# Kernel optimization log

Measured on AMD Instinct MI355X. Metric: run time of the kernel, lower is better.

## Reference

```python
import jax, jax.numpy as jnp
import numpy as np

D_MODEL = 1024
NUM_HEADS = 16
D_K = D_MODEL // NUM_HEADS
B, T = 2, 2048


def setup_inputs() -> dict:
    key = jax.random.key(0)
    ks = jax.random.split(key, 11)
    s = 1.0 / np.sqrt(D_MODEL)
    inp = {
        "q": jax.random.normal(ks[0], (B, T, D_MODEL), jnp.float32),
        "k": jax.random.normal(ks[1], (B, T, D_MODEL), jnp.float32),
        "v": jax.random.normal(ks[2], (B, T, D_MODEL), jnp.float32),
        "mask": jnp.tril(jnp.ones((1, 1, T, T), jnp.int32)),  # causal
        "wq": jax.random.normal(ks[3], (D_MODEL, D_MODEL), jnp.float32) * s,
        "bq": jnp.zeros((D_MODEL,), jnp.float32),
        "wk": jax.random.normal(ks[4], (D_MODEL, D_MODEL), jnp.float32) * s,
        "bk": jnp.zeros((D_MODEL,), jnp.float32),
        "wv": jax.random.normal(ks[5], (D_MODEL, D_MODEL), jnp.float32) * s,
        "bv": jnp.zeros((D_MODEL,), jnp.float32),
        "wo": jax.random.normal(ks[6], (D_MODEL, D_MODEL), jnp.float32) * s,
        "bo": jnp.zeros((D_MODEL,), jnp.float32),
    }
    return inp


def reference(q, k, v, mask, wq, bq, wk, bk, wv, bv, wo, bo):
    Bq, Tq, _ = q.shape
    Tk = k.shape[1]
    # projections, split into heads: (B, H, T, d_k)
    qh = (q @ wq + bq).reshape(Bq, Tq, NUM_HEADS, D_K).transpose(0, 2, 1, 3)
    kh = (k @ wk + bk).reshape(Bq, Tk, NUM_HEADS, D_K).transpose(0, 2, 1, 3)
    vh = (v @ wv + bv).reshape(Bq, Tk, NUM_HEADS, D_K).transpose(0, 2, 1, 3)
    scores = jnp.einsum("bhqd,bhkd->bhqk", qh, kh) / jnp.sqrt(jnp.float32(D_K))
    scores = jnp.where(mask == 0, jnp.float32(-1e9), scores)
    attn = jax.nn.softmax(scores, axis=-1)
    ctx = jnp.einsum("bhqk,bhkd->bhqd", attn, vh)
    ctx = ctx.transpose(0, 2, 1, 3).reshape(Bq, Tq, D_MODEL)
    return ctx @ wo + bo
```

## Files before the change

kernel.cpp:

```cpp
#include <hip/hip_runtime.h>
#include <hip/hip_bf16.h>

#define DM 1024
#define NH 16
#define DK 64
#define TT 2048
#define BATCH 2

typedef __attribute__((ext_vector_type(8))) short bf16x8;
typedef __attribute__((ext_vector_type(4))) float f32x4;
typedef __attribute__((ext_vector_type(4))) unsigned short u16x4;
typedef unsigned short u16;

__device__ inline u16 f2b(float x){ __hip_bfloat16 h = __float2bfloat16(x); return *reinterpret_cast<u16*>(&h); }

__device__ inline void gl_lds16(const u16* g, u16* l) {
  __builtin_amdgcn_global_load_lds(
      (const __attribute__((address_space(1))) unsigned int*)g,
      (__attribute__((address_space(3))) unsigned int*)l, 16, 0, 0);
}

__global__ __launch_bounds__(256) void prep(const float* __restrict__ q, const float* __restrict__ k,
                                            const float* __restrict__ v,
                                            const float* __restrict__ wq, const float* __restrict__ wk,
                                            const float* __restrict__ wv, const float* __restrict__ wo,
                                            u16* __restrict__ qb, u16* __restrict__ kb,
                                            u16* __restrict__ vb, u16* __restrict__ wt) {
  int z = blockIdx.z;
  if (z < 3) {
    const float* src = z==0 ? q : z==1 ? k : v;
    u16* dst = z==0 ? qb : z==1 ? kb : vb;
    size_t i = ((size_t)blockIdx.x*256 + threadIdx.x)*8;
    f32x4 a = *(const f32x4*)(src+i);
    f32x4 b = *(const f32x4*)(src+i+4);
    union { bf16x8 v8; u16 e[8]; } u;
    #pragma unroll
    for (int j=0;j<4;j++){ u.e[j] = f2b(a[j]); u.e[4+j] = f2b(b[j]); }
    *(bf16x8*)(dst+i) = u.v8;
  } else {
    int bx = blockIdx.x;
    if (bx >= 1024) return;
    __shared__ float tile[32][33];
    const float* src = z==3 ? wq : z==4 ? wk : z==5 ? wv : wo;
    u16* dst = wt + (size_t)(z-3)*DM*DM;
    int bxx = bx & 31, byy = bx >> 5;
    int tx = threadIdx.x & 31, ty = threadIdx.x >> 5;
    int x  = bxx*32 + tx;
    int y0 = byy*32 + ty;
    #pragma unroll
    for (int i=0;i<32;i+=8) tile[ty+i][tx] = src[(size_t)(y0+i)*DM + x];
    __syncthreads();
    int xo = byy*32 + tx;
    int yo = bxx*32 + ty;
    #pragma unroll
    for (int i=0;i<32;i+=8) dst[(size_t)(yo+i)*DM + xo] = f2b(tile[tx][ty+i]);
  }
}

__global__ __launch_bounds__(256) void gemm_qkv(const u16* __restrict__ qb, const u16* __restrict__ kb,
                                                const u16* __restrict__ vb, const u16* __restrict__ wt,
                                                const float* __restrict__ bq, const float* __restrict__ bk,
                                                const float* __restrict__ bv,
                                                u16* __restrict__ qh, u16* __restrict__ kh,
                                                u16* __restrict__ vhT) {
  const int z = blockIdx.z;
  const u16* A = z==0 ? qb : z==1 ? kb : vb;
  const u16* W = wt + (size_t)z*DM*DM;
  const float* bias = z==0 ? bq : z==1 ? bk : bv;
  u16* outv = z==0 ? qh : z==1 ? kh : vhT;
  const int mode = (z==2) ? 1 : 0;
  const float oscale = (z==0) ? 0.125f : 1.0f;

  __shared__ u16 As[2][128*32];
  __shared__ u16 Bs[2][128*32];
  const int tid = threadIdx.x, lane = tid & 63, wid = tid >> 6;
  const int li = lane & 15, quad = lane >> 4;
  const int row0 = blockIdx.x*128, col0 = blockIdx.y*128;
  const int wr = wid & 1, wc = wid >> 1;

  f32x4 acc[4][4];
  #pragma unroll
  for (int i=0;i<4;i++)
    #pragma unroll
    for (int j=0;j<4;j++) acc[i][j] = f32x4{0.f,0.f,0.f,0.f};

  const int srow = lane >> 2;
  const int scol = (lane & 3) * 8;

  for (int k0 = 0; k0 < DM; k0 += 64) {
    __syncthreads();
    #pragma unroll
    for (int s=0;s<2;s++)
      #pragma unroll
      for (int c=0;c<2;c++) {
        int ch = wid*2 + c;
        gl_lds16(A + (size_t)(row0 + ch*16 + srow)*DM + k0 + s*32 + scol, As[s] + ch*512);
        gl_lds16(W + (size_t)(col0 + ch*16 + srow)*DM + k0 + s*32 + scol, Bs[s] + ch*512);
      }
    __syncthreads();
    #pragma unroll
    for (int s=0;s<2;s++) {
      bf16x8 a[4], b[4];
      #pragma unroll
      for (int i=0;i<4;i++) a[i] = *(const bf16x8*)&As[s][(wr*64 + i*16 + li)*32 + quad*8];
      #pragma unroll
      for (int j=0;j<4;j++) b[j] = *(const bf16x8*)&Bs[s][(wc*64 + j*16 + li)*32 + quad*8];
      #pragma unroll
      for (int i=0;i<4;i++)
        #pragma unroll
        for (int j=0;j<4;j++)
          acc[i][j] = __builtin_amdgcn_mfma_f32_16x16x32_bf16(a[i], b[j], acc[i][j], 0,0,0);
    }
  }

  #pragma unroll
  for (int j=0;j<4;j++) {
    int col = col0 + wc*64 + j*16 + li;
    float bsv = bias[col];
    #pragma unroll
    for (int i=0;i<4;i++) {
      #pragma unroll
      for (int r=0;r<4;r++) {
        int row = row0 + wr*64 + i*16 + quad*4 + r;
        float vv = (acc[i][j][r] + bsv) * oscale;
        int bb = row >> 11, t = row & (TT-1);
        int hh = col >> 6,  d = col & 63;
        size_t idx = (mode == 0)
          ? ((((size_t)(bb*NH + hh)*TT + t) << 6) + d)
          : ((((size_t)(bb*NH + hh)*DK + d)*TT) + t);
        outv[idx] = f2b(vv);
      }
    }
  }
}

__global__ __launch_bounds__(256) void gemm_out64(const u16* __restrict__ A, const u16* __restrict__ W,
                                                  const float* __restrict__ bias, float* __restrict__ out) {
  __shared__ u16 As[2][128*32];
  __shared__ u16 Bs[2][64*32];
  const int tid = threadIdx.x, lane = tid & 63, wid = tid >> 6;
  const int li = lane & 15, quad = lane >> 4;
  const int row0 = blockIdx.x*128, col0 = blockIdx.y*64;
  const int wr = wid & 1, wc = wid >> 1;

  f32x4 acc[4][2];
  #pragma unroll
  for (int i=0;i<4;i++)
    #pragma unroll
    for (int j=0;j<2;j++) acc[i][j] = f32x4{0.f,0.f,0.f,0.f};

  const int srow = lane >> 2;
  const int scol = (lane & 3) * 8;

  for (int k0 = 0; k0 < DM; k0 += 64) {
    __syncthreads();
    #pragma unroll
    for (int s=0;s<2;s++) {
      #pragma unroll
      for (int c=0;c<2;c++) {
        int ch = wid*2 + c;
        gl_lds16(A + (size_t)(row0 + ch*16 + srow)*DM + k0 + s*32 + scol, As[s] + ch*512);
      }
      gl_lds16(W + (size_t)(col0 + wid*16 + srow)*DM + k0 + s*32 + scol, Bs[s] + wid*512);
    }
    __syncthreads();
    #pragma unroll
    for (int s=0;s<2;s++) {
      bf16x8 a[4], b[2];
      #pragma unroll
      for (int i=0;i<4;i++) a[i] = *(const bf16x8*)&As[s][(wr*64 + i*16 + li)*32 + quad*8];
      #pragma unroll
      for (int j=0;j<2;j++) b[j] = *(const bf16x8*)&Bs[s][(wc*32 + j*16 + li)*32 + quad*8];
      #pragma unroll
      for (int i=0;i<4;i++)
        #pragma unroll
        for (int j=0;j<2;j++)
          acc[i][j] = __builtin_amdgcn_mfma_f32_16x16x32_bf16(a[i], b[j], acc[i][j], 0,0,0);
    }
  }

  #pragma unroll
  for (int j=0;j<2;j++) {
    int col = col0 + wc*32 + j*16 + li;
    float bsv = bias[col];
    #pragma unroll
    for (int i=0;i<4;i++) {
      #pragma unroll
      for (int r=0;r<4;r++) {
        int row = row0 + wr*64 + i*16 + quad*4 + r;
        out[(size_t)row*DM + col] = acc[i][j][r] + bsv;
      }
    }
  }
}

__global__ __launch_bounds__(256) void flash(const u16* __restrict__ qh, const u16* __restrict__ kh,
                                             const u16* __restrict__ vhT, u16* __restrict__ ctx) {
  const int bh = blockIdx.x;
  const int pr = blockIdx.y;
  const int b = bh >> 4, h = bh & 15;
  const u16* Q  = qh  + (size_t)bh*TT*DK;
  const u16* K  = kh  + (size_t)bh*TT*DK;
  const u16* Vt = vhT + (size_t)bh*DK*TT;

  const int tid = threadIdx.x, lane = tid & 63, wid = tid >> 6;
  const int li = lane & 15, quad = lane >> 4;

  __shared__ u16 Kl[64][72];
  __shared__ u16 Vl[64][72];
  __shared__ u16 Pb[4][16][72];

  const int sr = tid >> 3;
  const int sc = (tid & 7) * 8;

  bf16x8 kr0 = *(const bf16x8*)&K[(size_t)(sr   )*DK + sc];
  bf16x8 kr1 = *(const bf16x8*)&K[(size_t)(sr+32)*DK + sc];
  bf16x8 vr0 = *(const bf16x8*)&Vt[(size_t)(sr   )*TT + sc];
  bf16x8 vr1 = *(const bf16x8*)&Vt[(size_t)(sr+32)*TT + sc];

  #pragma unroll
  for (int ph = 0; ph < 2; ph++) {
    const int qt = (ph == 0) ? pr : (31 - pr);
    const int nt = qt + 1;
    const int qrow0 = qt*64 + wid*16;

    bf16x8 qf0 = *(const bf16x8*)&Q[(size_t)(qrow0+li)*DK +      quad*8];
    bf16x8 qf1 = *(const bf16x8*)&Q[(size_t)(qrow0+li)*DK + 32 + quad*8];

    f32x4 o[4];
    #pragma unroll
    for (int d=0;d<4;d++) o[d] = f32x4{0.f,0.f,0.f,0.f};
    float lp = 0.f;

    for (int it = 0; it < nt; it++) {
      const int k0 = it*64;
      __syncthreads();
      *(bf16x8*)&Kl[sr   ][sc] = kr0;
      *(bf16x8*)&Kl[sr+32][sc] = kr1;
      *(bf16x8*)&Vl[sr   ][sc] = vr0;
      *(bf16x8*)&Vl[sr+32][sc] = vr1;
      __syncthreads();
      if (it+1 < nt) {
        const int k1 = k0 + 64;
        kr0 = *(const bf16x8*)&K[(size_t)(k1+sr   )*DK + sc];
        kr1 = *(const bf16x8*)&K[(size_t)(k1+sr+32)*DK + sc];
        vr0 = *(const bf16x8*)&Vt[(size_t)(sr   )*TT + k1 + sc];
        vr1 = *(const bf16x8*)&Vt[(size_t)(sr+32)*TT + k1 + sc];
      } else if (ph == 0) {
        kr0 = *(const bf16x8*)&K[(size_t)(sr   )*DK + sc];
        kr1 = *(const bf16x8*)&K[(size_t)(sr+32)*DK + sc];
        vr0 = *(const bf16x8*)&Vt[(size_t)(sr   )*TT + sc];
        vr1 = *(const bf16x8*)&Vt[(size_t)(sr+32)*TT + sc];
      }

      f32x4 s[4];
      #pragma unroll
      for (int c=0;c<4;c++) {
        bf16x8 kf0 = *(const bf16x8*)&Kl[c*16+li][     quad*8];
        bf16x8 kf1 = *(const bf16x8*)&Kl[c*16+li][32 + quad*8];
        f32x4 t = __builtin_amdgcn_mfma_f32_16x16x32_bf16(kf0, qf0, f32x4{0.f,0.f,0.f,0.f}, 0,0,0);
        s[c]    = __builtin_amdgcn_mfma_f32_16x16x32_bf16(kf1, qf1, t, 0,0,0);
      }
      const bool dg = (it == nt-1);
      const int qq = qrow0 + li;
      float p[4][4];
      if (dg) {
        #pragma unroll
        for (int c=0;c<4;c++)
          #pragma unroll
          for (int r=0;r<4;r++){
            int key = k0 + c*16 + quad*4 + r;
            p[c][r] = (key <= qq) ? __expf(s[c][r]) : 0.f;
          }
      } else {
        #pragma unroll
        for (int c=0;c<4;c++)
          #pragma unroll
          for (int r=0;r<4;r++)
            p[c][r] = __expf(s[c][r]);
      }
      #pragma unroll
      for (int c=0;c<4;c++)
        #pragma unroll
        for (int r=0;r<4;r++)
          lp += p[c][r];

      #pragma unroll
      for (int c=0;c<4;c++) {
        u16x4 w;
        #pragma unroll
        for (int r=0;r<4;r++) w[r] = f2b(p[c][r]);
        *(u16x4*)&Pb[wid][li][c*16 + quad*4] = w;
      }
      __builtin_amdgcn_wave_barrier();
      __asm__ __volatile__("s_waitcnt lgkmcnt(0)");
      bf16x8 pf0 = *(const bf16x8*)&Pb[wid][li][     quad*8];
      bf16x8 pf1 = *(const bf16x8*)&Pb[wid][li][32 + quad*8];

      #pragma unroll
      for (int d=0;d<4;d++){
        bf16x8 vf0 = *(const bf16x8*)&Vl[d*16+li][     quad*8];
        bf16x8 vf1 = *(const bf16x8*)&Vl[d*16+li][32 + quad*8];
        o[d] = __builtin_amdgcn_mfma_f32_16x16x32_bf16(vf0, pf0, o[d], 0,0,0);
        o[d] = __builtin_amdgcn_mfma_f32_16x16x32_bf16(vf1, pf1, o[d], 0,0,0);
      }
    }

    lp += __shfl_xor(lp, 16, 64);
    lp += __shfl_xor(lp, 32, 64);
    float rl = 1.0f / lp;

    const int qq = qrow0 + li;
    #pragma unroll
    for (int d=0;d<4;d++){
      u16x4 w;
      #pragma unroll
      for (int r=0;r<4;r++) w[r] = f2b(o[d][r] * rl);
      *(u16x4*)&ctx[(size_t)(b*TT + qq)*DM + h*DK + d*16 + quad*4] = w;
    }
  }
}

extern "C" void kernel_launch(void* const* d_in, const int* in_sizes, int n_in,
                              void* d_out, int out_size, void* d_ws, size_t ws_size,
                              hipStream_t stream) {
  const float* q   = (const float*)d_in[0];
  const float* k   = (const float*)d_in[1];
  const float* v   = (const float*)d_in[2];
  const float* wq  = (const float*)d_in[4];
  const float* bq  = (const float*)d_in[5];
  const float* wk  = (const float*)d_in[6];
  const float* bk  = (const float*)d_in[7];
  const float* wv  = (const float*)d_in[8];
  const float* bv  = (const float*)d_in[9];
  const float* wo  = (const float*)d_in[10];
  const float* bo  = (const float*)d_in[11];
  float* out = (float*)d_out;

  const size_t SZ = (size_t)BATCH*TT*DM;
  u16* wt  = (u16*)d_ws;
  u16* qb  = wt + (size_t)4*DM*DM;
  u16* kb  = qb + SZ;
  u16* vb  = kb + SZ;
  u16* qh  = vb + SZ;
  u16* kh  = qh + SZ;
  u16* vhT = kh + SZ;
  u16* ctx = qb;

  prep<<<dim3(2048, 1, 7), 256, 0, stream>>>(q, k, v, wq, wk, wv, wo, qb, kb, vb, wt);

  gemm_qkv<<<dim3(4096/128, DM/128, 3), 256, 0, stream>>>(qb, kb, vb, wt, bq, bk, bv, qh, kh, vhT);

  flash<<<dim3(BATCH*NH, 16), 256, 0, stream>>>(qh, kh, vhT, ctx);

  gemm_out64<<<dim3(4096/128, DM/64), 256, 0, stream>>>(ctx, wt + (size_t)3*DM*DM, bo, out);
}
```

Measured before the change: 236.8 us.

## Double-buffer flash K/V tiles in one merged loop; shrink QKV GEMM k-step

The flash kernel now runs both causal query tiles as one flat 33-iteration loop. K/V tiles are double-buffered in LDS, so each tile is written to the other buffer after the compute and one barrier per iteration is dropped. The QKV GEMM drops its two-stage 64-wide k-chunk for a single 32-wide LDS stage, with loads issued before the barrier. That halves GEMM shared memory but doubles the number of barriers and shortens each compute burst, which may hurt the GEMM.

```diff
diff --git a/kernel.cpp b/kernel.cpp
--- a/kernel.cpp
+++ b/kernel.cpp
@@ -71,8 +71,8 @@
   const int mode = (z==2) ? 1 : 0;
   const float oscale = (z==0) ? 0.125f : 1.0f;
 
-  __shared__ u16 As[2][128*32];
-  __shared__ u16 Bs[2][128*32];
+  __shared__ u16 As[128*32];
+  __shared__ u16 Bs[128*32];
   const int tid = threadIdx.x, lane = tid & 63, wid = tid >> 6;
   const int li = lane & 15, quad = lane >> 4;
   const int row0 = blockIdx.x*128, col0 = blockIdx.y*128;
@@ -87,30 +87,25 @@
   const int srow = lane >> 2;
   const int scol = (lane & 3) * 8;
 
-  for (int k0 = 0; k0 < DM; k0 += 64) {
-    __syncthreads();
-    #pragma unroll
-    for (int s=0;s<2;s++)
-      #pragma unroll
-      for (int c=0;c<2;c++) {
-        int ch = wid*2 + c;
-        gl_lds16(A + (size_t)(row0 + ch*16 + srow)*DM + k0 + s*32 + scol, As[s] + ch*512);
-        gl_lds16(W + (size_t)(col0 + ch*16 + srow)*DM + k0 + s*32 + scol, Bs[s] + ch*512);
-      }
-    __syncthreads();
-    #pragma unroll
-    for (int s=0;s<2;s++) {
-      bf16x8 a[4], b[4];
-      #pragma unroll
-      for (int i=0;i<4;i++) a[i] = *(const bf16x8*)&As[s][(wr*64 + i*16 + li)*32 + quad*8];
-      #pragma unroll
-      for (int j=0;j<4;j++) b[j] = *(const bf16x8*)&Bs[s][(wc*64 + j*16 + li)*32 + quad*8];
-      #pragma unroll
-      for (int i=0;i<4;i++)
-        #pragma unroll
-        for (int j=0;j<4;j++)
-          acc[i][j] = __builtin_amdgcn_mfma_f32_16x16x32_bf16(a[i], b[j], acc[i][j], 0,0,0);
-    }
+  for (int k0 = 0; k0 < DM; k0 += 32) {
+    #pragma unroll
+    for (int c = 0; c < 2; c++) {
+      int ch = wid*2 + c;
+      gl_lds16(A + (size_t)(row0 + ch*16 + srow)*DM + k0 + scol, As + ch*512);
+      gl_lds16(W + (size_t)(col0 + ch*16 + srow)*DM + k0 + scol, Bs + ch*512);
+    }
+    __syncthreads();
+    bf16x8 a[4], b[4];
+    #pragma unroll
+    for (int i=0;i<4;i++) a[i] = *(const bf16x8*)&As[(wr*64 + i*16 + li)*32 + quad*8];
+    #pragma unroll
+    for (int j=0;j<4;j++) b[j] = *(const bf16x8*)&Bs[(wc*64 + j*16 + li)*32 + quad*8];
+    #pragma unroll
+    for (int i=0;i<4;i++)
+      #pragma unroll
+      for (int j=0;j<4;j++)
+        acc[i][j] = __builtin_amdgcn_mfma_f32_16x16x32_bf16(a[i], b[j], acc[i][j], 0,0,0);
+    __syncthreads();
   }
 
   #pragma unroll
@@ -206,118 +201,146 @@
   const int tid = threadIdx.x, lane = tid & 63, wid = tid >> 6;
   const int li = lane & 15, quad = lane >> 4;
 
-  __shared__ u16 Kl[64][72];
-  __shared__ u16 Vl[64][72];
+  __shared__ u16 Kl[2][64][72];
+  __shared__ u16 Vl[2][64][72];
   __shared__ u16 Pb[4][16][72];
 
   const int sr = tid >> 3;
   const int sc = (tid & 7) * 8;
+
+  const int ntA = pr + 1;
+  const int qrA = pr*64 + wid*16;
+  const int qrB = (31-pr)*64 + wid*16;
+
+  bf16x8 qfA0 = *(const bf16x8*)&Q[(size_t)(qrA+li)*DK +      quad*8];
+  bf16x8 qfA1 = *(const bf16x8*)&Q[(size_t)(qrA+li)*DK + 32 + quad*8];
+  bf16x8 qfB0 = *(const bf16x8*)&Q[(size_t)(qrB+li)*DK +      quad*8];
+  bf16x8 qfB1 = *(const bf16x8*)&Q[(size_t)(qrB+li)*DK + 32 + quad*8];
 
   bf16x8 kr0 = *(const bf16x8*)&K[(size_t)(sr   )*DK + sc];
   bf16x8 kr1 = *(const bf16x8*)&K[(size_t)(sr+32)*DK + sc];
   bf16x8 vr0 = *(const bf16x8*)&Vt[(size_t)(sr   )*TT + sc];
   bf16x8 vr1 = *(const bf16x8*)&Vt[(size_t)(sr+32)*TT + sc];
-
-  #pragma unroll
-  for (int ph = 0; ph < 2; ph++) {
-    const int qt = (ph == 0) ? pr : (31 - pr);
-    const int nt = qt + 1;
-    const int qrow0 = qt*64 + wid*16;
-
-    bf16x8 qf0 = *(const bf16x8*)&Q[(size_t)(qrow0+li)*DK +      quad*8];
-    bf16x8 qf1 = *(const bf16x8*)&Q[(size_t)(qrow0+li)*DK + 32 + quad*8];
-
-    f32x4 o[4];
-    #pragma unroll
-    for (int d=0;d<4;d++) o[d] = f32x4{0.f,0.f,0.f,0.f};
-    float lp = 0.f;
-
-    for (int it = 0; it < nt; it++) {
-      const int k0 = it*64;
-      __syncthreads();
-      *(bf16x8*)&Kl[sr   ][sc] = kr0;
-      *(bf16x8*)&Kl[sr+32][sc] = kr1;
-      *(bf16x8*)&Vl[sr   ][sc] = vr0;
-      *(bf16x8*)&Vl[sr+32][sc] = vr1;
-      __syncthreads();
-      if (it+1 < nt) {
-        const int k1 = k0 + 64;
-        kr0 = *(const bf16x8*)&K[(size_t)(k1+sr   )*DK + sc];
-        kr1 = *(const bf16x8*)&K[(size_t)(k1+sr+32)*DK + sc];
-        vr0 = *(const bf16x8*)&Vt[(size_t)(sr   )*TT + k1 + sc];
-        vr1 = *(const bf16x8*)&Vt[(size_t)(sr+32)*TT + k1 + sc];
-      } else if (ph == 0) {
-        kr0 = *(const bf16x8*)&K[(size_t)(sr   )*DK + sc];
-        kr1 = *(const bf16x8*)&K[(size_t)(sr+32)*DK + sc];
-        vr0 = *(const bf16x8*)&Vt[(size_t)(sr   )*TT + sc];
-        vr1 = *(const bf16x8*)&Vt[(size_t)(sr+32)*TT + sc];
-      }
-
-      f32x4 s[4];
-      #pragma unroll
-      for (int c=0;c<4;c++) {
-        bf16x8 kf0 = *(const bf16x8*)&Kl[c*16+li][     quad*8];
-        bf16x8 kf1 = *(const bf16x8*)&Kl[c*16+li][32 + quad*8];
-        f32x4 t = __builtin_amdgcn_mfma_f32_16x16x32_bf16(kf0, qf0, f32x4{0.f,0.f,0.f,0.f}, 0,0,0);
-        s[c]    = __builtin_amdgcn_mfma_f32_16x16x32_bf16(kf1, qf1, t, 0,0,0);
-      }
-      const bool dg = (it == nt-1);
-      const int qq = qrow0 + li;
-      float p[4][4];
-      if (dg) {
+  *(bf16x8*)&Kl[0][sr   ][sc] = kr0;
+  *(bf16x8*)&Kl[0][sr+32][sc] = kr1;
+  *(bf16x8*)&Vl[0][sr   ][sc] = vr0;
+  *(bf16x8*)&Vl[0][sr+32][sc] = vr1;
+  {
+    const int kn = (1 < ntA) ? 64 : 0;
+    kr0 = *(const bf16x8*)&K[(size_t)(kn+sr   )*DK + sc];
+    kr1 = *(const bf16x8*)&K[(size_t)(kn+sr+32)*DK + sc];
+    vr0 = *(const bf16x8*)&Vt[(size_t)(sr   )*TT + kn + sc];
+    vr1 = *(const bf16x8*)&Vt[(size_t)(sr+32)*TT + kn + sc];
+  }
+
+  f32x4 o[4];
+  #pragma unroll
+  for (int d=0;d<4;d++) o[d] = f32x4{0.f,0.f,0.f,0.f};
+  float lp = 0.f;
+  int qrow0 = qrA;
+  bf16x8 qf0 = qfA0, qf1 = qfA1;
+  int cur = 0;
+
+  for (int g = 0; g < 33; g++) {
+    __syncthreads();
+    const int k0 = ((g < ntA) ? g : (g - ntA)) * 64;
+    const bool dg = (g == ntA-1) || (g == 32);
+
+    f32x4 s[4];
+    #pragma unroll
+    for (int c=0;c<4;c++) {
+      bf16x8 kf0 = *(const bf16x8*)&Kl[cur][c*16+li][     quad*8];
+      bf16x8 kf1 = *(const bf16x8*)&Kl[cur][c*16+li][32 + quad*8];
+      f32x4 t = __builtin_amdgcn_mfma_f32_16x16x32_bf16(kf0, qf0, f32x4{0.f,0.f,0.f,0.f}, 0,0,0);
+      s[c]    = __builtin_amdgcn_mfma_f32_16x16x32_bf16(kf1, qf1, t, 0,0,0);
+    }
+    const int qq = qrow0 + li;
+    float p[4][4];
+    if (dg) {
+      #pragma unroll
+      for (int c=0;c<4;c++)
         #pragma unroll
-        for (int c=0;c<4;c++)
-          #pragma unroll
-          for (int r=0;r<4;r++){
-            int key = k0 + c*16 + quad*4 + r;
-            p[c][r] = (key <= qq) ? __expf(s[c][r]) : 0.f;
-          }
-      } else {
-        #pragma unroll
-        for (int c=0;c<4;c++)
-          #pragma unroll
-          for (int r=0;r<4;r++)
-            p[c][r] = __expf(s[c][r]);
-      }
+        for (int r=0;r<4;r++){
+          int key = k0 + c*16 + quad*4 + r;
+          p[c][r] = (key <= qq) ? __expf(s[c][r]) : 0.f;
+        }
+    } else {
       #pragma unroll
       for (int c=0;c<4;c++)
         #pragma unroll
         for (int r=0;r<4;r++)
-          lp += p[c][r];
-
-      #pragma unroll
-      for (int c=0;c<4;c++) {
+          p[c][r] = __expf(s[c][r]);
+    }
+    #pragma unroll
+    for (int c=0;c<4;c++)
+      #pragma unroll
+      for (int r=0;r<4;r++)
+        lp += p[c][r];
+
+    #pragma unroll
+    for (int c=0;c<4;c++) {
+      u16x4 w;
+      #pragma unroll
+      for (int r=0;r<4;r++) w[r] = f2b(p[c][r]);
+      *(u16x4*)&Pb[wid][li][c*16 + quad*4] = w;
+    }
+    __builtin_amdgcn_wave_barrier();
+    __asm__ __volatile__("s_waitcnt lgkmcnt(0)");
+    bf16x8 pf0 = *(const bf16x8*)&Pb[wid][li][     quad*8];
+    bf16x8 pf1 = *(const bf16x8*)&Pb[wid][li][32 + quad*8];
+
+    #pragma unroll
+    for (int d=0;d<4;d++){
+      bf16x8 vf0 = *(const bf16x8*)&Vl[cur][d*16+li][     quad*8];
+      bf16x8 vf1 = *(const bf16x8*)&Vl[cur][d*16+li][32 + quad*8];
+      o[d] = __builtin_amdgcn_mfma_f32_16x16x32_bf16(vf0, pf0, o[d], 0,0,0);
+      o[d] = __builtin_amdgcn_mfma_f32_16x16x32_bf16(vf1, pf1, o[d], 0,0,0);
+    }
+
+    if (g + 1 < 33) {
+      *(bf16x8*)&Kl[cur^1][sr   ][sc] = kr0;
+      *(bf16x8*)&Kl[cur^1][sr+32][sc] = kr1;
+      *(bf16x8*)&Vl[cur^1][sr   ][sc] = vr0;
+      *(bf16x8*)&Vl[cur^1][sr+32][sc] = vr1;
+      if (g + 2 < 33) {
+        const int g2 = g + 2;
+        const int kn = ((g2 < ntA) ? g2 : (g2 - ntA)) * 64;
+        kr0 = *(const bf16x8*)&K[(size_t)(kn+sr   )*DK + sc];
+        kr1 = *(const bf16x8*)&K[(size_t)(kn+sr+32)*DK + sc];
+        vr0 = *(const bf16x8*)&Vt[(size_t)(sr   )*TT + kn + sc];
+        vr1 = *(const bf16x8*)&Vt[(size_t)(sr+32)*TT + kn + sc];
+      }
+    }
+    cur ^= 1;
+
+    if (g == ntA-1) {
+      float l = lp;
+      l += __shfl_xor(l, 16, 64);
+      l += __shfl_xor(l, 32, 64);
+      float rl = 1.0f / l;
+      #pragma unroll
+      for (int d=0;d<4;d++){
         u16x4 w;
         #pragma unroll
-        for (int r=0;r<4;r++) w[r] = f2b(p[c][r]);
-        *(u16x4*)&Pb[wid][li][c*16 + quad*4] = w;
-      }
-      __builtin_amdgcn_wave_barrier();
-      __asm__ __volatile__("s_waitcnt lgkmcnt(0)");
-      bf16x8 pf0 = *(const bf16x8*)&Pb[wid][li][     quad*8];
-      bf16x8 pf1 = *(const bf16x8*)&Pb[wid][li][32 + quad*8];
-
-      #pragma unroll
-      for (int d=0;d<4;d++){
-        bf16x8 vf0 = *(const bf16x8*)&Vl[d*16+li][     quad*8];
-        bf16x8 vf1 = *(const bf16x8*)&Vl[d*16+li][32 + quad*8];
-        o[d] = __builtin_amdgcn_mfma_f32_16x16x32_bf16(vf0, pf0, o[d], 0,0,0);
-        o[d] = __builtin_amdgcn_mfma_f32_16x16x32_bf16(vf1, pf1, o[d], 0,0,0);
-      }
-    }
-
-    lp += __shfl_xor(lp, 16, 64);
-    lp += __shfl_xor(lp, 32, 64);
-    float rl = 1.0f / lp;
-
-    const int qq = qrow0 + li;
-    #pragma unroll
-    for (int d=0;d<4;d++){
-      u16x4 w;
-      #pragma unroll
-      for (int r=0;r<4;r++) w[r] = f2b(o[d][r] * rl);
-      *(u16x4*)&ctx[(size_t)(b*TT + qq)*DM + h*DK + d*16 + quad*4] = w;
-    }
+        for (int r=0;r<4;r++) w[r] = f2b(o[d][r] * rl);
+        *(u16x4*)&ctx[(size_t)(b*TT + qrA + li)*DM + h*DK + d*16 + quad*4] = w;
+      }
+      #pragma unroll
+      for (int d=0;d<4;d++) o[d] = f32x4{0.f,0.f,0.f,0.f};
+      lp = 0.f;
+      qrow0 = qrB; qf0 = qfB0; qf1 = qfB1;
+    }
+  }
+
+  lp += __shfl_xor(lp, 16, 64);
+  lp += __shfl_xor(lp, 32, 64);
+  float rl = 1.0f / lp;
+  #pragma unroll
+  for (int d=0;d<4;d++){
+    u16x4 w;
+    #pragma unroll
+    for (int r=0;r<4;r++) w[r] = f2b(o[d][r] * rl);
+    *(u16x4*)&ctx[(size_t)(b*TT + qrB + li)*DM + h*DK + d*16 + quad*4] = w;
   }
 }
 
```

Result: slower. 241.8 us (+2.1%).
